# Kernel optimization log

Measured on AMD Instinct MI355X. Metric: run time of the kernel, lower is better.

The kernel has to match this reference:

```python
import jax, jax.numpy as jnp
import numpy as np

BN_EPS = 1e-5
N_IN, N_OUT = 200000, 400000
K, M, C_IN, C_OUT = 27, 100000, 64, 64


def setup_inputs() -> dict:
    key = jax.random.key(0)
    ks = jax.random.split(key, 4)
    x = jax.random.normal(ks[0], (N_IN, C_IN), dtype=jnp.float32)
    W = jax.random.normal(ks[1], (K, C_IN, C_OUT), dtype=jnp.float32) * 0.05
    gamma = jnp.ones((C_OUT,), dtype=jnp.float32)
    beta = jnp.zeros((C_OUT,), dtype=jnp.float32)
    in_idx = jax.random.randint(ks[2], (K, M), 0, N_IN, dtype=jnp.int32)
    out_idx = jax.random.randint(ks[3], (K, M), 0, N_OUT, dtype=jnp.int32)
    return {"x": x, "W": W, "gamma": gamma, "beta": beta,
            "in_idx": in_idx, "out_idx": out_idx, "n_out": N_OUT}


def reference(x, W, gamma, beta, in_idx, out_idx, n_out):
    # Sparse transposed conv via gather-GEMM-scatter over K kernel offsets.
    feats = x[in_idx]                               # [K, M, C_in] gather
    contrib = jnp.einsum('kmi,kio->kmo', feats, W)  # per-offset GEMM
    out = jnp.zeros((n_out, contrib.shape[-1]), dtype=x.dtype)
    out = out.at[out_idx.reshape(-1)].add(contrib.reshape(-1, contrib.shape[-1]))
    # BatchNorm (training-mode batch stats over all output points), gamma=1, beta=0 at init.
    mean = jnp.mean(out, axis=0)
    var = jnp.var(out, axis=0)
    y = (out - mean) * jax.lax.rsqrt(var + BN_EPS) * gamma + beta
    return jax.nn.relu(y)
```

## Files before the change

### kernel.cpp

```cpp
#include <hip/hip_runtime.h>

#define K_OFF 27
#define M_PTS 100000
#define C_CH 64
#define N_OUT_PTS 400000
#define BN_EPS 1e-5f
#define PTS_PER_WAVE 50

__global__ __launch_bounds__(256, 2) void scatter_gemm(
    const float* __restrict__ x, const float* __restrict__ W,
    const int* __restrict__ in_idx, const int* __restrict__ out_idx,
    float* __restrict__ out_ws)
{
    const int k = blockIdx.y;
    const int lane = threadIdx.x & 63;
    const int wave = __builtin_amdgcn_readfirstlane(threadIdx.x >> 6);

    const float* __restrict__ Wk = W + (size_t)k * C_CH * C_CH;
    float w[C_CH];
    #pragma unroll
    for (int i = 0; i < C_CH; ++i) w[i] = Wk[i * C_CH + lane];

    const int m0 = (blockIdx.x * 4 + wave) * PTS_PER_WAVE;
    const int base = k * M_PTS + m0;

    const int li = lane < PTS_PER_WAVE ? lane : PTS_PER_WAVE - 1;
    const int vsrc = in_idx[base + li];
    const int vdst = out_idx[base + li];

    float4 u[16], v[16];
    {
        int s0 = __builtin_amdgcn_readlane(vsrc, 0);
        const float4* xr = (const float4*)(x + (size_t)s0 * C_CH);
        #pragma unroll
        for (int j = 0; j < 16; ++j) u[j] = xr[j];
        int s1 = __builtin_amdgcn_readlane(vsrc, 1);
        const float4* xs = (const float4*)(x + (size_t)s1 * C_CH);
        #pragma unroll
        for (int j = 0; j < 16; ++j) v[j] = xs[j];
    }

    for (int p = 0; p < PTS_PER_WAVE; p += 2) {
        {
            float a0 = 0.f, a1 = 0.f;
            #pragma unroll
            for (int j = 0; j < 16; j += 2) {
                float4 t0 = u[j], t1 = u[j + 1];
                a0 = fmaf(t0.x, w[4 * j + 0], a0);
                a0 = fmaf(t0.y, w[4 * j + 1], a0);
                a0 = fmaf(t0.z, w[4 * j + 2], a0);
                a0 = fmaf(t0.w, w[4 * j + 3], a0);
                a1 = fmaf(t1.x, w[4 * j + 4], a1);
                a1 = fmaf(t1.y, w[4 * j + 5], a1);
                a1 = fmaf(t1.z, w[4 * j + 6], a1);
                a1 = fmaf(t1.w, w[4 * j + 7], a1);
            }
            int dst = __builtin_amdgcn_readlane(vdst, p);
            unsafeAtomicAdd(&out_ws[(size_t)dst * C_CH + lane], a0 + a1);
        }
        {
            int pn = (p + 2 < PTS_PER_WAVE) ? p + 2 : PTS_PER_WAVE - 1;
            int sn = __builtin_amdgcn_readlane(vsrc, pn);
            const float4* xr = (const float4*)(x + (size_t)sn * C_CH);
            #pragma unroll
            for (int j = 0; j < 16; ++j) u[j] = xr[j];
        }
        {
            float a0 = 0.f, a1 = 0.f;
            #pragma unroll
            for (int j = 0; j < 16; j += 2) {
                float4 t0 = v[j], t1 = v[j + 1];
                a0 = fmaf(t0.x, w[4 * j + 0], a0);
                a0 = fmaf(t0.y, w[4 * j + 1], a0);
                a0 = fmaf(t0.z, w[4 * j + 2], a0);
                a0 = fmaf(t0.w, w[4 * j + 3], a0);
                a1 = fmaf(t1.x, w[4 * j + 4], a1);
                a1 = fmaf(t1.y, w[4 * j + 5], a1);
                a1 = fmaf(t1.z, w[4 * j + 6], a1);
                a1 = fmaf(t1.w, w[4 * j + 7], a1);
            }
            int dst = __builtin_amdgcn_readlane(vdst, p + 1);
            unsafeAtomicAdd(&out_ws[(size_t)dst * C_CH + lane], a0 + a1);
        }
        {
            int pn = (p + 3 < PTS_PER_WAVE) ? p + 3 : PTS_PER_WAVE - 1;
            int sn = __builtin_amdgcn_readlane(vsrc, pn);
            const float4* xs = (const float4*)(x + (size_t)sn * C_CH);
            #pragma unroll
            for (int j = 0; j < 16; ++j) v[j] = xs[j];
        }
    }
}

__global__ __launch_bounds__(256) void bn_stats(
    const float* __restrict__ ws, float* __restrict__ stats)
{
    const float4* in4 = (const float4*)ws;
    const size_t n4 = (size_t)N_OUT_PTS * C_CH / 4;
    const size_t stride = (size_t)gridDim.x * blockDim.x;
    float s[4] = {0, 0, 0, 0}, s2[4] = {0, 0, 0, 0};
    for (size_t i = (size_t)blockIdx.x * blockDim.x + threadIdx.x; i < n4; i += stride) {
        float4 t = in4[i];
        s[0] += t.x; s2[0] += t.x * t.x;
        s[1] += t.y; s2[1] += t.y * t.y;
        s[2] += t.z; s2[2] += t.z * t.z;
        s[3] += t.w; s2[3] += t.w * t.w;
    }
    __shared__ float sh[2][256][4];
    #pragma unroll
    for (int j = 0; j < 4; ++j) { sh[0][threadIdx.x][j] = s[j]; sh[1][threadIdx.x][j] = s2[j]; }
    __syncthreads();
    if (threadIdx.x < C_CH) {
        const int c = threadIdx.x;
        float ts = 0.f, t2 = 0.f;
        #pragma unroll
        for (int j = 0; j < 16; ++j) {
            ts += sh[0][(c >> 2) + 16 * j][c & 3];
            t2 += sh[1][(c >> 2) + 16 * j][c & 3];
        }
        unsafeAtomicAdd(&stats[c], ts);
        unsafeAtomicAdd(&stats[C_CH + c], t2);
    }
}

__global__ __launch_bounds__(256) void bn_apply(
    const float* __restrict__ ws, const float* __restrict__ stats,
    const float* __restrict__ gamma, const float* __restrict__ beta,
    float* __restrict__ out)
{
    const float inv_n = 1.0f / (float)N_OUT_PTS;
    const int c0 = (threadIdx.x * 4) & 63;
    float sc[4], bs[4];
    #pragma unroll
    for (int j = 0; j < 4; ++j) {
        int c = c0 + j;
        float mean = stats[c] * inv_n;
        float var = stats[C_CH + c] * inv_n - mean * mean;
        float s = gamma[c] * rsqrtf(var + BN_EPS);
        sc[j] = s;
        bs[j] = beta[c] - mean * s;
    }
    const float4* in4 = (const float4*)ws;
    float4* o4 = (float4*)out;
    const size_t n4 = (size_t)N_OUT_PTS * C_CH / 4;
    const size_t stride = (size_t)gridDim.x * blockDim.x;
    for (size_t i = (size_t)blockIdx.x * blockDim.x + threadIdx.x; i < n4; i += stride) {
        float4 v = in4[i];
        v.x = fmaxf(fmaf(v.x, sc[0], bs[0]), 0.f);
        v.y = fmaxf(fmaf(v.y, sc[1], bs[1]), 0.f);
        v.z = fmaxf(fmaf(v.z, sc[2], bs[2]), 0.f);
        v.w = fmaxf(fmaf(v.w, sc[3], bs[3]), 0.f);
        o4[i] = v;
    }
}

extern "C" void kernel_launch(void* const* d_in, const int* in_sizes, int n_in,
                              void* d_out, int out_size, void* d_ws, size_t ws_size,
                              hipStream_t stream) {
    const float* x      = (const float*)d_in[0];
    const float* W      = (const float*)d_in[1];
    const float* gamma  = (const float*)d_in[2];
    const float* beta   = (const float*)d_in[3];
    const int*   in_idx = (const int*)d_in[4];
    const int*   out_idx= (const int*)d_in[5];
    float* out = (float*)d_out;

    float* out_ws = (float*)d_ws;
    float* stats  = out_ws + (size_t)N_OUT_PTS * C_CH;

    const size_t acc_bytes = (size_t)N_OUT_PTS * C_CH * sizeof(float) + 2 * C_CH * sizeof(float);
    hipMemsetAsync(d_ws, 0, acc_bytes, stream);

    dim3 g1(M_PTS / (4 * PTS_PER_WAVE), K_OFF);
    scatter_gemm<<<g1, 256, 0, stream>>>(x, W, in_idx, out_idx, out_ws);

    bn_stats<<<2048, 256, 0, stream>>>(out_ws, stats);

    bn_apply<<<2048, 256, 0, stream>>>(out_ws, stats, gamma, beta, out);
}
```

Before: 839.8 us.

## Accumulate scatter output in bf16 using packed atomic adds

Switches the scatter accumulation buffer from fp32 to bf16. Each wave pairs adjacent channels with shuffles and issues half as many global_atomic_pk_add_bf16 operations, and the BN stats and apply kernels read packed bf16. This halves atomic traffic and workspace bandwidth. In exchange, summing up to many contributions per output in bf16 loses a lot of precision, which can break tolerance checks.

```diff
diff --git a/kernel.cpp b/kernel.cpp
--- a/kernel.cpp
+++ b/kernel.cpp
@@ -1,4 +1,5 @@
 #include <hip/hip_runtime.h>
+#include <hip/hip_bf16.h>
 
 #define K_OFF 27
 #define M_PTS 100000
@@ -7,10 +8,23 @@
 #define BN_EPS 1e-5f
 #define PTS_PER_WAVE 50
 
+__device__ inline void pk_atomic_add_bf16(__hip_bfloat16* p, int bits) {
+#if __has_builtin(__builtin_amdgcn_global_atomic_fadd_v2bf16)
+    typedef short s2v __attribute__((ext_vector_type(2)));
+    typedef __attribute__((address_space(1))) s2v* gp;
+    s2v v;
+    __builtin_memcpy(&v, &bits, 4);
+    __builtin_amdgcn_global_atomic_fadd_v2bf16((gp)(unsigned long long)p, v);
+#else
+    asm volatile("global_atomic_pk_add_bf16 %0, %1, off"
+                 :: "v"((unsigned long long)p), "v"(bits) : "memory");
+#endif
+}
+
 __global__ __launch_bounds__(256, 2) void scatter_gemm(
     const float* __restrict__ x, const float* __restrict__ W,
     const int* __restrict__ in_idx, const int* __restrict__ out_idx,
-    float* __restrict__ out_ws)
+    __hip_bfloat16* __restrict__ out_ws)
 {
     const int k = blockIdx.y;
     const int lane = threadIdx.x & 63;
@@ -39,6 +53,8 @@
         #pragma unroll
         for (int j = 0; j < 16; ++j) v[j] = xs[j];
     }
+
+    const int pl = lane & 31;
 
     for (int p = 0; p < PTS_PER_WAVE; p += 2) {
         {
@@ -55,8 +71,15 @@
                 a1 = fmaf(t1.z, w[4 * j + 6], a1);
                 a1 = fmaf(t1.w, w[4 * j + 7], a1);
             }
+            float val = a0 + a1;
             int dst = __builtin_amdgcn_readlane(vdst, p);
-            unsafeAtomicAdd(&out_ws[(size_t)dst * C_CH + lane], a0 + a1);
+            float lo = __shfl(val, 2 * pl);
+            float hi = __shfl(val, 2 * pl + 1);
+            if (lane < 32) {
+                union { __hip_bfloat162 h; int i; } cv;
+                cv.h = __hip_bfloat162(__float2bfloat16(lo), __float2bfloat16(hi));
+                pk_atomic_add_bf16(out_ws + (size_t)dst * C_CH + 2 * lane, cv.i);
+            }
         }
         {
             int pn = (p + 2 < PTS_PER_WAVE) ? p + 2 : PTS_PER_WAVE - 1;
@@ -79,8 +102,15 @@
                 a1 = fmaf(t1.z, w[4 * j + 6], a1);
                 a1 = fmaf(t1.w, w[4 * j + 7], a1);
             }
+            float val = a0 + a1;
             int dst = __builtin_amdgcn_readlane(vdst, p + 1);
-            unsafeAtomicAdd(&out_ws[(size_t)dst * C_CH + lane], a0 + a1);
+            float lo = __shfl(val, 2 * pl);
+            float hi = __shfl(val, 2 * pl + 1);
+            if (lane < 32) {
+                union { __hip_bfloat162 h; int i; } cv;
+                cv.h = __hip_bfloat162(__float2bfloat16(lo), __float2bfloat16(hi));
+                pk_atomic_add_bf16(out_ws + (size_t)dst * C_CH + 2 * lane, cv.i);
+            }
         }
         {
             int pn = (p + 3 < PTS_PER_WAVE) ? p + 3 : PTS_PER_WAVE - 1;
@@ -93,30 +123,36 @@
 }
 
 __global__ __launch_bounds__(256) void bn_stats(
-    const float* __restrict__ ws, float* __restrict__ stats)
+    const __hip_bfloat16* __restrict__ ws, float* __restrict__ stats)
 {
-    const float4* in4 = (const float4*)ws;
-    const size_t n4 = (size_t)N_OUT_PTS * C_CH / 4;
+    const uint4* in = (const uint4*)ws;
+    const size_t n = (size_t)N_OUT_PTS * C_CH / 8;
     const size_t stride = (size_t)gridDim.x * blockDim.x;
-    float s[4] = {0, 0, 0, 0}, s2[4] = {0, 0, 0, 0};
-    for (size_t i = (size_t)blockIdx.x * blockDim.x + threadIdx.x; i < n4; i += stride) {
-        float4 t = in4[i];
-        s[0] += t.x; s2[0] += t.x * t.x;
-        s[1] += t.y; s2[1] += t.y * t.y;
-        s[2] += t.z; s2[2] += t.z * t.z;
-        s[3] += t.w; s2[3] += t.w * t.w;
-    }
-    __shared__ float sh[2][256][4];
-    #pragma unroll
-    for (int j = 0; j < 4; ++j) { sh[0][threadIdx.x][j] = s[j]; sh[1][threadIdx.x][j] = s2[j]; }
+    float s[8], s2[8];
+    #pragma unroll
+    for (int j = 0; j < 8; ++j) { s[j] = 0.f; s2[j] = 0.f; }
+    for (size_t i = (size_t)blockIdx.x * blockDim.x + threadIdx.x; i < n; i += stride) {
+        uint4 q = in[i];
+        unsigned wds[4] = {q.x, q.y, q.z, q.w};
+        #pragma unroll
+        for (int j = 0; j < 4; ++j) {
+            __hip_bfloat162 h = *(__hip_bfloat162*)&wds[j];
+            float f0 = __low2float(h), f1 = __high2float(h);
+            s[2 * j] += f0;  s2[2 * j] += f0 * f0;
+            s[2 * j + 1] += f1; s2[2 * j + 1] += f1 * f1;
+        }
+    }
+    __shared__ float sh[2][256][8];
+    #pragma unroll
+    for (int j = 0; j < 8; ++j) { sh[0][threadIdx.x][j] = s[j]; sh[1][threadIdx.x][j] = s2[j]; }
     __syncthreads();
     if (threadIdx.x < C_CH) {
         const int c = threadIdx.x;
         float ts = 0.f, t2 = 0.f;
         #pragma unroll
-        for (int j = 0; j < 16; ++j) {
-            ts += sh[0][(c >> 2) + 16 * j][c & 3];
-            t2 += sh[1][(c >> 2) + 16 * j][c & 3];
+        for (int q = 0; q < 32; ++q) {
+            ts += sh[0][8 * q + (c >> 3)][c & 7];
+            t2 += sh[1][8 * q + (c >> 3)][c & 7];
         }
         unsafeAtomicAdd(&stats[c], ts);
         unsafeAtomicAdd(&stats[C_CH + c], t2);
@@ -124,15 +160,15 @@
 }
 
 __global__ __launch_bounds__(256) void bn_apply(
-    const float* __restrict__ ws, const float* __restrict__ stats,
+    const __hip_bfloat16* __restrict__ ws, const float* __restrict__ stats,
     const float* __restrict__ gamma, const float* __restrict__ beta,
     float* __restrict__ out)
 {
     const float inv_n = 1.0f / (float)N_OUT_PTS;
-    const int c0 = (threadIdx.x * 4) & 63;
-    float sc[4], bs[4];
-    #pragma unroll
-    for (int j = 0; j < 4; ++j) {
+    const int c0 = 8 * (threadIdx.x & 7);
+    float sc[8], bs[8];
+    #pragma unroll
+    for (int j = 0; j < 8; ++j) {
         int c = c0 + j;
         float mean = stats[c] * inv_n;
         float var = stats[C_CH + c] * inv_n - mean * mean;
@@ -140,17 +176,31 @@
         sc[j] = s;
         bs[j] = beta[c] - mean * s;
     }
-    const float4* in4 = (const float4*)ws;
+    const uint4* in = (const uint4*)ws;
     float4* o4 = (float4*)out;
-    const size_t n4 = (size_t)N_OUT_PTS * C_CH / 4;
+    const size_t n = (size_t)N_OUT_PTS * C_CH / 8;
     const size_t stride = (size_t)gridDim.x * blockDim.x;
-    for (size_t i = (size_t)blockIdx.x * blockDim.x + threadIdx.x; i < n4; i += stride) {
-        float4 v = in4[i];
-        v.x = fmaxf(fmaf(v.x, sc[0], bs[0]), 0.f);
-        v.y = fmaxf(fmaf(v.y, sc[1], bs[1]), 0.f);
-        v.z = fmaxf(fmaf(v.z, sc[2], bs[2]), 0.f);
-        v.w = fmaxf(fmaf(v.w, sc[3], bs[3]), 0.f);
-        o4[i] = v;
+    for (size_t i = (size_t)blockIdx.x * blockDim.x + threadIdx.x; i < n; i += stride) {
+        uint4 q = in[i];
+        unsigned wds[4] = {q.x, q.y, q.z, q.w};
+        float f[8];
+        #pragma unroll
+        for (int j = 0; j < 4; ++j) {
+            __hip_bfloat162 h = *(__hip_bfloat162*)&wds[j];
+            f[2 * j] = __low2float(h);
+            f[2 * j + 1] = __high2float(h);
+        }
+        float4 r0, r1;
+        r0.x = fmaxf(fmaf(f[0], sc[0], bs[0]), 0.f);
+        r0.y = fmaxf(fmaf(f[1], sc[1], bs[1]), 0.f);
+        r0.z = fmaxf(fmaf(f[2], sc[2], bs[2]), 0.f);
+        r0.w = fmaxf(fmaf(f[3], sc[3], bs[3]), 0.f);
+        r1.x = fmaxf(fmaf(f[4], sc[4], bs[4]), 0.f);
+        r1.y = fmaxf(fmaf(f[5], sc[5], bs[5]), 0.f);
+        r1.z = fmaxf(fmaf(f[6], sc[6], bs[6]), 0.f);
+        r1.w = fmaxf(fmaf(f[7], sc[7], bs[7]), 0.f);
+        o4[2 * i] = r0;
+        o4[2 * i + 1] = r1;
     }
 }
 
@@ -165,11 +215,12 @@
     const int*   out_idx= (const int*)d_in[5];
     float* out = (float*)d_out;
 
-    float* out_ws = (float*)d_ws;
-    float* stats  = out_ws + (size_t)N_OUT_PTS * C_CH;
-
-    const size_t acc_bytes = (size_t)N_OUT_PTS * C_CH * sizeof(float) + 2 * C_CH * sizeof(float);
-    hipMemsetAsync(d_ws, 0, acc_bytes, stream);
+    __hip_bfloat16* out_ws = (__hip_bfloat16*)d_ws;
+    const size_t acc_elems = (size_t)N_OUT_PTS * C_CH;
+    float* stats = (float*)((char*)d_ws + acc_elems * sizeof(__hip_bfloat16));
+
+    const size_t clear_bytes = acc_elems * sizeof(__hip_bfloat16) + 2 * C_CH * sizeof(float);
+    (void)hipMemsetAsync(d_ws, 0, clear_bytes, stream);
 
     dim3 g1(M_PTS / (4 * PTS_PER_WAVE), K_OFF);
     scatter_gemm<<<g1, 256, 0, stream>>>(x, W, in_idx, out_idx, out_ws);
```

Result: faster. 706.5 us (-15.9%).
